# Performance work log

Hardware: AMD Instinct MI355X
Metric: run time of the kernel (lower is better)

Reference implementation:

```python
import jax, jax.numpy as jnp
import numpy as np

EMBED_DIM = 1024
NHEAD = 16
HEAD_DIM = EMBED_DIM // NHEAD
BASE = 10000.0


def rope_tables(seq_len, dim):
    # dim = head_dim; freqs over dim/2
    inv_freq = 1.0 / (BASE ** (jnp.arange(0, dim, 2, dtype=jnp.float32) / dim))
    t = jnp.arange(seq_len, dtype=jnp.float32)
    freqs = jnp.einsum('i,j->ij', t, inv_freq)          # [S, dim/2]
    return jnp.cos(freqs), jnp.sin(freqs)


def apply_rope(x, cos, sin):
    # x: [B,H,S,D]; cos/sin: [S, D/2] broadcast over B,H
    x1, x2 = jnp.split(x, 2, axis=-1)
    return jnp.concatenate((x1 * cos - x2 * sin, x1 * sin + x2 * cos), axis=-1)


def setup_inputs() -> dict:
    key = jax.random.key(0)
    ks = jax.random.split(key, 7)
    B, S, E = 2, 2048, EMBED_DIM
    scale = 1.0 / np.sqrt(E)
    return {
        'query': jax.random.normal(ks[0], (B, S, E), dtype=jnp.float32),
        'key':   jax.random.normal(ks[1], (B, S, E), dtype=jnp.float32),
        'value': jax.random.normal(ks[2], (B, S, E), dtype=jnp.float32),
        'Wq': jax.random.normal(ks[3], (E, E), dtype=jnp.float32) * scale,
        'Wk': jax.random.normal(ks[4], (E, E), dtype=jnp.float32) * scale,
        'Wv': jax.random.normal(ks[5], (E, E), dtype=jnp.float32) * scale,
        'Wo': jax.random.normal(ks[6], (E, E), dtype=jnp.float32) * scale,
    }


def reference(query, key, value, Wq, Wk, Wv, Wo):
    B, Sq, E = query.shape
    Skv = key.shape[1]
    H, D = NHEAD, HEAD_DIM
    # projections (nn.Linear: x @ W.T), split heads -> [B,H,S,D]
    q = (query @ Wq.T).reshape(B, Sq, H, D).transpose(0, 2, 1, 3)
    k = (key   @ Wk.T).reshape(B, Skv, H, D).transpose(0, 2, 1, 3)
    v = (value @ Wv.T).reshape(B, Skv, H, D).transpose(0, 2, 1, 3)
    cos, sin = rope_tables(Sq, D)
    q = apply_rope(q, cos, sin)
    k = apply_rope(k, cos, sin)
    scores = jnp.einsum('bhqd,bhkd->bhqk', q, k) / jnp.sqrt(jnp.asarray(D, q.dtype))
    probs = jax.nn.softmax(scores, axis=-1)
    out = jnp.einsum('bhqk,bhkd->bhqd', probs, v)
    out = out.transpose(0, 2, 1, 3).reshape(B, Sq, E)
    return out @ Wo.T
```

## Files before the change

kernel.cpp:

```cpp
#include <hip/hip_runtime.h>

typedef __bf16 bf16_t;
typedef __attribute__((ext_vector_type(8))) __bf16 bf16x8;
typedef __attribute__((ext_vector_type(4))) __bf16 bf16x4;
typedef __attribute__((ext_vector_type(4))) float f32x4;
typedef __attribute__((ext_vector_type(16))) float f32x16;
typedef __attribute__((ext_vector_type(4))) int i32x4;

#define GAS __attribute__((address_space(1)))
#define LAS __attribute__((address_space(3)))

#define CFENCE() asm volatile("" ::: "memory")

__device__ __forceinline__ void gload_lds16(const bf16_t* g, bf16_t* l) {
  __builtin_amdgcn_global_load_lds((const GAS char*)(const char*)g,
                                   (LAS char*)(char*)l, 16, 0, 0);
}

__global__ __launch_bounds__(256) void f2bf_w(const float* __restrict__ wq,
                                              const float* __restrict__ wk,
                                              const float* __restrict__ wv,
                                              const float* __restrict__ wo,
                                              bf16_t* __restrict__ wsb,
                                              float* __restrict__ ct,
                                              float* __restrict__ st) {
  if (blockIdx.x >= 4096) {
    const int gid = (blockIdx.x - 4096) * 256 + threadIdx.x;
    const int s = gid >> 5, j = gid & 31;
    const float inv = exp2f(-(float)j * (13.287712379549449f / 32.0f));
    const float ang = (float)s * inv;
    ct[gid] = cosf(ang);
    st[gid] = sinf(ang);
    return;
  }
  const size_t W = 1048576;
  const size_t gid = (size_t)(blockIdx.x * 256 + threadIdx.x) * 4;
  const float* src; size_t off;
  if      (gid < W)     { src = wq; off = gid; }
  else if (gid < 2 * W) { src = wk; off = gid - W; }
  else if (gid < 3 * W) { src = wv; off = gid - 2 * W; }
  else                  { src = wo; off = gid - 3 * W; }
  const float4 vv = *(const float4*)(src + off);
  bf16x4 o;
  o[0] = (bf16_t)vv.x; o[1] = (bf16_t)vv.y; o[2] = (bf16_t)vv.z; o[3] = (bf16_t)vv.w;
  *(bf16x4*)(wsb + gid) = o;
}

template <int EPI, int AF32>
__device__ __forceinline__ void gemm_bt_body(const void* __restrict__ Ap,
                                             const bf16_t* __restrict__ Bm,
                                             void* __restrict__ Cout,
                                             const float* __restrict__ ctab,
                                             const float* __restrict__ stab,
                                             const float scale,
                                             const int m0, const int n0,
                                             bf16_t* __restrict__ sm) {
  constexpr int K = 1024, N = 1024;
  bf16_t* As = sm;
  bf16_t* Bs0 = sm + 8192;
  const int tid = threadIdx.x;
  const int lane = tid & 63;
  const int w = tid >> 6;
  const int wr = w >> 1, wc = w & 1;
  const int g = lane >> 4, c = lane & 15;
  const bf16_t* Ab = (const bf16_t*)Ap;
  const float* Af = (const float*)Ap;

  f32x4 acc[4][4] = {};

  if (AF32) {
    float4 aregs[2][8];
#pragma unroll
    for (int i = 0; i < 4; ++i) {
      const int chunk0 = (i * 4 + w) * 64;
      const int idx = chunk0 + lane;
      const int row = idx >> 3;
      const int sw = (idx & 7) ^ (row & 7);
      gload_lds16(Bm + (size_t)(n0 + row) * K + sw * 8, Bs0 + chunk0 * 8);
    }
    CFENCE();
#pragma unroll
    for (int i = 0; i < 4; ++i) {
      const int idx8 = i * 256 + tid;
      const int row = idx8 >> 3, j8 = idx8 & 7;
      const size_t base = (size_t)(m0 + row) * K + j8 * 8;
      aregs[0][2 * i]     = *(const float4*)(Af + base);
      aregs[0][2 * i + 1] = *(const float4*)(Af + base + 4);
    }
    CFENCE();
#pragma unroll
    for (int i = 0; i < 4; ++i) {
      const int idx8 = i * 256 + tid;
      const int row = idx8 >> 3, j8 = idx8 & 7;
      const size_t base = (size_t)(m0 + row) * K + 64 + j8 * 8;
      aregs[1][2 * i]     = *(const float4*)(Af + base);
      aregs[1][2 * i + 1] = *(const float4*)(Af + base + 4);
    }
    asm volatile("s_waitcnt vmcnt(8)" ::: "memory");

#pragma unroll
    for (int t = 0; t < 16; ++t) {
      const int pc = t & 1;
      bf16_t* BsC = Bs0 + pc * 8192;
      bf16_t* BsN = Bs0 + (pc ^ 1) * 8192;
      if (t > 0) { __builtin_amdgcn_s_barrier(); CFENCE(); }
#pragma unroll
      for (int i = 0; i < 4; ++i) {
        const int idx8 = i * 256 + tid;
        const int row = idx8 >> 3, j8 = idx8 & 7;
        bf16x8 o;
        o[0] = (bf16_t)aregs[pc][2 * i].x;     o[1] = (bf16_t)aregs[pc][2 * i].y;
        o[2] = (bf16_t)aregs[pc][2 * i].z;     o[3] = (bf16_t)aregs[pc][2 * i].w;
        o[4] = (bf16_t)aregs[pc][2 * i + 1].x; o[5] = (bf16_t)aregs[pc][2 * i + 1].y;
        o[6] = (bf16_t)aregs[pc][2 * i + 1].z; o[7] = (bf16_t)aregs[pc][2 * i + 1].w;
        *(bf16x8*)(As + row * 64 + ((j8 ^ (row & 7)) * 8)) = o;
      }
      CFENCE();
      if (t < 15) {
#pragma unroll
        for (int i = 0; i < 4; ++i) {
          const int chunk0 = (i * 4 + w) * 64;
          const int idx = chunk0 + lane;
          const int row = idx >> 3;
          const int sw = (idx & 7) ^ (row & 7);
          gload_lds16(Bm + (size_t)(n0 + row) * K + ((t + 1) * 64 + sw * 8),
                      BsN + chunk0 * 8);
        }
      }
      CFENCE();
      if (t < 14) {
#pragma unroll
        for (int i = 0; i < 4; ++i) {
          const int idx8 = i * 256 + tid;
          const int row = idx8 >> 3, j8 = idx8 & 7;
          const size_t base = (size_t)(m0 + row) * K + (t + 2) * 64 + j8 * 8;
          aregs[pc][2 * i]     = *(const float4*)(Af + base);
          aregs[pc][2 * i + 1] = *(const float4*)(Af + base + 4);
        }
      }
      asm volatile("s_waitcnt lgkmcnt(0)" ::: "memory");
      __builtin_amdgcn_s_barrier();
      CFENCE();
      bf16x8 af[4][2], bfr[4][2];
#pragma unroll
      for (int tt = 0; tt < 4; ++tt)
#pragma unroll
        for (int kc = 0; kc < 2; ++kc) {
          const int ra = wr * 64 + tt * 16 + c;
          af[tt][kc] = *(const bf16x8*)(As + ra * 64 + (((kc * 4 + g) ^ (ra & 7)) * 8));
          const int rb = wc * 64 + tt * 16 + c;
          bfr[tt][kc] = *(const bf16x8*)(BsC + rb * 64 + (((kc * 4 + g) ^ (rb & 7)) * 8));
        }
#pragma unroll
      for (int mi = 0; mi < 4; ++mi)
#pragma unroll
        for (int ni = 0; ni < 4; ++ni)
#pragma unroll
          for (int kc = 0; kc < 2; ++kc)
            acc[mi][ni] = __builtin_amdgcn_mfma_f32_16x16x32_bf16(
                af[mi][kc], bfr[ni][kc], acc[mi][ni], 0, 0, 0);
      if (t < 14)       asm volatile("s_waitcnt vmcnt(8)" ::: "memory");
      else if (t == 14) asm volatile("s_waitcnt vmcnt(0)" ::: "memory");
    }
    __syncthreads();
  } else {
    for (int k0 = 0; k0 < K; k0 += 64) {
#pragma unroll
      for (int i = 0; i < 4; ++i) {
        const int chunk0 = (i * 4 + w) * 64;
        const int idx = chunk0 + lane;
        const int row = idx >> 3;
        const int sw = (idx & 7) ^ (row & 7);
        gload_lds16(Ab + (size_t)(m0 + row) * K + (k0 + sw * 8), As + chunk0 * 8);
        gload_lds16(Bm + (size_t)(n0 + row) * K + (k0 + sw * 8), Bs0 + chunk0 * 8);
      }
      __syncthreads();
      bf16x8 af[4][2], bfr[4][2];
#pragma unroll
      for (int tt = 0; tt < 4; ++tt)
#pragma unroll
        for (int kc = 0; kc < 2; ++kc) {
          const int ra = wr * 64 + tt * 16 + c;
          af[tt][kc] = *(const bf16x8*)(As + ra * 64 + (((kc * 4 + g) ^ (ra & 7)) * 8));
          const int rb = wc * 64 + tt * 16 + c;
          bfr[tt][kc] = *(const bf16x8*)(Bs0 + rb * 64 + (((kc * 4 + g) ^ (rb & 7)) * 8));
        }
#pragma unroll
      for (int mi = 0; mi < 4; ++mi)
#pragma unroll
        for (int ni = 0; ni < 4; ++ni)
#pragma unroll
          for (int kc = 0; kc < 2; ++kc)
            acc[mi][ni] = __builtin_amdgcn_mfma_f32_16x16x32_bf16(
                af[mi][kc], bfr[ni][kc], acc[mi][ni], 0, 0, 0);
      __syncthreads();
    }
  }

  if (EPI == 2) {
#pragma unroll
    for (int mi = 0; mi < 4; ++mi)
#pragma unroll
      for (int ni = 0; ni < 4; ++ni)
#pragma unroll
        for (int r = 0; r < 4; ++r) {
          const int lr = wr * 64 + mi * 16 + g * 4 + r;
          const int lc = wc * 64 + ni * 16 + c;
          sm[lc * 136 + lr] = (bf16_t)acc[mi][ni][r];
        }
    __syncthreads();
    bf16_t* Vt = (bf16_t*)Cout;
    const int bb = m0 >> 11, sbase = m0 & 2047;
#pragma unroll
    for (int it = 0; it < 8; ++it) {
      const int idx = it * 256 + tid;
      const int lc = idx >> 4, kk = idx & 15;
      const bf16x8 vv = *(const bf16x8*)(sm + lc * 136 + kk * 8);
      *(bf16x8*)(Vt + ((size_t)(bb * 1024 + n0 + lc)) * 2048 + sbase + kk * 8) = vv;
    }
    return;
  }
  if (EPI == 0 && ctab != nullptr) {
    bf16_t* Cb = (bf16_t*)Cout;
#pragma unroll
    for (int mi = 0; mi < 4; ++mi)
#pragma unroll
      for (int r = 0; r < 4; ++r) {
        const int grow = m0 + wr * 64 + mi * 16 + g * 4 + r;
        const int s = grow & 2047;
        const float* crow = ctab + s * 32;
        const float* srow = stab + s * 32;
#pragma unroll
        for (int ni = 0; ni < 2; ++ni) {
          const int j = ni * 16 + c;
          const float cc = crow[j], ss = srow[j];
          const float x1 = acc[mi][ni][r];
          const float x2 = acc[mi][ni + 2][r];
          const int gcol = n0 + wc * 64 + j;
          Cb[(size_t)grow * N + gcol]      = (bf16_t)((x1 * cc - x2 * ss) * scale);
          Cb[(size_t)grow * N + gcol + 32] = (bf16_t)((x1 * ss + x2 * cc) * scale);
        }
      }
    return;
  }
#pragma unroll
  for (int mi = 0; mi < 4; ++mi)
#pragma unroll
    for (int ni = 0; ni < 4; ++ni)
#pragma unroll
      for (int r = 0; r < 4; ++r) {
        const int grow = m0 + wr * 64 + mi * 16 + g * 4 + r;
        const int gcol = n0 + wc * 64 + ni * 16 + c;
        const float v = acc[mi][ni][r];
        if (EPI == 0) ((bf16_t*)Cout)[(size_t)grow * N + gcol] = (bf16_t)v;
        else          ((float*)Cout)[(size_t)grow * N + gcol] = v;
      }
}

__global__ __launch_bounds__(256) void qkv_gemm(
    const float* __restrict__ qf, const float* __restrict__ kf, const float* __restrict__ vf,
    const bf16_t* __restrict__ wqb, const bf16_t* __restrict__ wkb, const bf16_t* __restrict__ wvb,
    bf16_t* __restrict__ Qp, bf16_t* __restrict__ Kp, bf16_t* __restrict__ Vtp,
    const float* __restrict__ ctab, const float* __restrict__ stab) {
  __shared__ __align__(16) bf16_t sm[24576];
  const int bid = blockIdx.x;
  const int wg = (bid & 7) * 96 + (bid >> 3);
  const int z = wg >> 8;
  const int rem = wg & 255;
  const int m0 = (rem >> 3) * 128;
  const int n0 = (rem & 7) * 128;
  if (z == 0) {
    gemm_bt_body<0, 1>(qf, wqb, Qp, ctab, stab, 0.18033688011112042f, m0, n0, sm);
  } else if (z == 1) {
    gemm_bt_body<0, 1>(kf, wkb, Kp, ctab, stab, 1.0f, m0, n0, sm);
  } else {
    gemm_bt_body<2, 1>(vf, wvb, Vtp, nullptr, nullptr, 1.0f, m0, n0, sm);
  }
}

__global__ __launch_bounds__(256) void out_gemm(const bf16_t* __restrict__ A,
                                                const bf16_t* __restrict__ B,
                                                float* __restrict__ C) {
  __shared__ __align__(16) bf16_t sm[17408];
  const int bid = blockIdx.x;
  const int wg = (bid & 7) * 32 + (bid >> 3);
  const int m0 = (wg >> 3) * 128;
  const int n0 = (wg & 7) * 128;
  gemm_bt_body<1, 0>(A, B, C, nullptr, nullptr, 1.0f, m0, n0, sm);
}

__global__ __launch_bounds__(512, 4) void flash_attn(const bf16_t* __restrict__ Q,
                                                     const bf16_t* __restrict__ Kr,
                                                     const bf16_t* __restrict__ Vt,
                                                     bf16_t* __restrict__ O) {
  __shared__ __align__(16) bf16_t Ksm[2][2][64 * 64];
  __shared__ __align__(16) bf16_t Vsm[2][2][64 * 64];
  const int tid = threadIdx.x, lane = tid & 63, w = tid >> 6;
  const int wl = w & 3, g = w >> 2;
  const int li = lane & 31, hi = lane >> 5;
  const int bid = blockIdx.x;
  const int xcd = bid & 7, slot = bid >> 3;
  const int bh = xcd * 4 + (slot >> 4);
  const int qb = slot & 15;
  const int b = bh >> 4, h = bh & 15;
  const int q0 = qb * 128 + wl * 32;

  bf16x8 qf[4];
  {
    const size_t qaddr = ((size_t)b * 2048 + q0 + li) * 1024 + h * 64 + hi * 8;
#pragma unroll
    for (int ks = 0; ks < 4; ++ks) qf[ks] = *(const bf16x8*)(Q + qaddr + ks * 16);
  }

  bf16x8 ones;
#pragma unroll
  for (int j = 0; j < 8; ++j) ones[j] = (bf16_t)1.0f;

  const f32x16 zero16 = {};
  f32x16 o0 = zero16, o1 = zero16, osum = zero16;

  const size_t kbase  = (size_t)b * 2048 * 1024 + h * 64;
  const size_t vtbase = (size_t)((b * 16 + h) * 64) * 2048;
  const int kv_off = g * 1024;

#define STAGE(buf, kv0)                                                          \
  {                                                                              \
    _Pragma("unroll")                                                            \
    for (int i = 0; i < 2; ++i) {                                                \
      const int chunk0 = (i * 4 + wl) * 64;                                      \
      const int idx = chunk0 + lane;                                             \
      const int row = idx >> 3;                                                  \
      const int sw = ((idx & 7) ^ (row & 7)) * 8;                                \
      gload_lds16(Kr + kbase + (size_t)((kv0) + row) * 1024 + sw,                \
                  &Ksm[g][buf][chunk0 * 8]);                                     \
      gload_lds16(Vt + vtbase + (size_t)row * 2048 + (kv0) + sw,                 \
                  &Vsm[g][buf][chunk0 * 8]);                                     \
    }                                                                            \
  }

#define CVTPK(dst, lo_, hi_) \
  asm("v_cvt_pk_bf16_f32 %0, %1, %2" : "=v"(dst) : "v"(lo_), "v"(hi_))
#define PLSWAP(x_, y_) \
  asm volatile("v_permlane32_swap_b32 %0, %1" : "+v"(x_), "+v"(y_))

  STAGE(0, kv_off)
  asm volatile("s_waitcnt vmcnt(0)" ::: "memory");
  __builtin_amdgcn_s_barrier();
  int cur = 0;
  for (int t = 0; t < 16; ++t) {
    if (t < 15) STAGE(cur ^ 1, kv_off + (t + 1) * 64)

    f32x16 p0 = zero16, p1 = zero16;
    __builtin_amdgcn_s_setprio(1);
#pragma unroll
    for (int ks = 0; ks < 4; ++ks) {
      const int r0 = li;
      const bf16x8 kf0 = *(const bf16x8*)(&Ksm[g][cur][r0 * 64 + (((ks * 2 + hi) ^ (r0 & 7)) * 8)]);
      p0 = __builtin_amdgcn_mfma_f32_32x32x16_bf16(kf0, qf[ks], p0, 0, 0, 0);
      const int r1 = 32 + li;
      const bf16x8 kf1 = *(const bf16x8*)(&Ksm[g][cur][r1 * 64 + (((ks * 2 + hi) ^ (r1 & 7)) * 8)]);
      p1 = __builtin_amdgcn_mfma_f32_32x32x16_bf16(kf1, qf[ks], p1, 0, 0, 0);
    }
    __builtin_amdgcn_s_setprio(0);

#pragma unroll
    for (int j = 0; j < 16; ++j) { p0[j] = exp2f(p0[j]); p1[j] = exp2f(p1[j]); }

    bf16x8 pa[4];
#pragma unroll
    for (int ks = 0; ks < 4; ++ks) {
      int A_, B_, C_, D_;
      if (ks == 0) { CVTPK(A_, p0[0], p0[1]); CVTPK(B_, p0[2], p0[3]);
                     CVTPK(C_, p0[4], p0[5]); CVTPK(D_, p0[6], p0[7]); }
      else if (ks == 1) { CVTPK(A_, p0[8],  p0[9]);  CVTPK(B_, p0[10], p0[11]);
                          CVTPK(C_, p0[12], p0[13]); CVTPK(D_, p0[14], p0[15]); }
      else if (ks == 2) { CVTPK(A_, p1[0], p1[1]); CVTPK(B_, p1[2], p1[3]);
                          CVTPK(C_, p1[4], p1[5]); CVTPK(D_, p1[6], p1[7]); }
      else { CVTPK(A_, p1[8],  p1[9]);  CVTPK(B_, p1[10], p1[11]);
             CVTPK(C_, p1[12], p1[13]); CVTPK(D_, p1[14], p1[15]); }
      PLSWAP(A_, C_);
      PLSWAP(B_, D_);
      i32x4 iv; iv[0] = A_; iv[1] = B_; iv[2] = C_; iv[3] = D_;
      pa[ks] = __builtin_bit_cast(bf16x8, iv);
    }

    __builtin_amdgcn_s_setprio(1);
#pragma unroll
    for (int ks = 0; ks < 4; ++ks) {
      const int r0 = li;
      const bf16x8 vf0 = *(const bf16x8*)(&Vsm[g][cur][r0 * 64 + (((ks * 2 + hi) ^ (r0 & 7)) * 8)]);
      o0 = __builtin_amdgcn_mfma_f32_32x32x16_bf16(pa[ks], vf0, o0, 0, 0, 0);
      const int r1 = 32 + li;
      const bf16x8 vf1 = *(const bf16x8*)(&Vsm[g][cur][r1 * 64 + (((ks * 2 + hi) ^ (r1 & 7)) * 8)]);
      o1 = __builtin_amdgcn_mfma_f32_32x32x16_bf16(pa[ks], vf1, o1, 0, 0, 0);
      osum = __builtin_amdgcn_mfma_f32_32x32x16_bf16(pa[ks], ones, osum, 0, 0, 0);
    }
    __builtin_amdgcn_s_setprio(0);

    if (t < 15) {
      asm volatile("s_waitcnt vmcnt(0)" ::: "memory");
      __builtin_amdgcn_s_barrier();
    }
    cur ^= 1;
  }
#undef STAGE
#undef CVTPK
#undef PLSWAP

  float* Osm = (float*)&Ksm[0][0][0];
  float* lsm = (float*)&Vsm[0][0][0];

  if (g == 1) {
    float* Ow = Osm + wl * 2048;
#pragma unroll
    for (int reg = 0; reg < 16; ++reg) {
      const int ql = (reg & 3) + 8 * (reg >> 2) + 4 * hi;
      Ow[ql * 64 + li]      = o0[reg];
      Ow[ql * 64 + 32 + li] = o1[reg];
      if (li == 0) lsm[wl * 32 + ql] = osum[reg];
    }
  }
  __syncthreads();
  if (g == 0) {
    const float* Ow = Osm + wl * 2048;
#pragma unroll
    for (int reg = 0; reg < 16; ++reg) {
      const int ql = (reg & 3) + 8 * (reg >> 2) + 4 * hi;
      const float rl = 1.0f / (osum[reg] + lsm[wl * 32 + ql]);
      const size_t base = ((size_t)b * 2048 + q0 + ql) * 1024 + h * 64 + li;
      O[base]      = (bf16_t)((o0[reg] + Ow[ql * 64 + li])      * rl);
      O[base + 32] = (bf16_t)((o1[reg] + Ow[ql * 64 + 32 + li]) * rl);
    }
  }
}

extern "C" void kernel_launch(void* const* d_in, const int* in_sizes, int n_in,
                              void* d_out, int out_size, void* d_ws, size_t ws_size,
                              hipStream_t stream) {
  (void)in_sizes; (void)n_in; (void)out_size; (void)ws_size;
  const float* q_in = (const float*)d_in[0];
  const float* k_in = (const float*)d_in[1];
  const float* v_in = (const float*)d_in[2];
  const float* wq = (const float*)d_in[3];
  const float* wk = (const float*)d_in[4];
  const float* wv = (const float*)d_in[5];
  const float* wo = (const float*)d_in[6];
  float* out = (float*)d_out;

  bf16_t* ws = (bf16_t*)d_ws;
  const size_t T = 4096ull * 1024ull;
  const size_t W = 1024ull * 1024ull;
  bf16_t* wqb = ws;
  bf16_t* wkb = wqb + W;
  bf16_t* wvb = wkb + W;
  bf16_t* wob = wvb + W;
  bf16_t* Qp  = wob + W;
  bf16_t* Kp  = Qp + T;
  bf16_t* Vtp = Kp + T;
  bf16_t* AO  = Vtp + T;
  float* ctab = (float*)(AO + T);
  float* stab = ctab + 65536;

  f2bf_w<<<4352, 256, 0, stream>>>(wq, wk, wv, wo, wqb, ctab, stab);
  qkv_gemm<<<768, 256, 0, stream>>>(q_in, k_in, v_in, wqb, wkb, wvb, Qp, Kp, Vtp,
                                    ctab, stab);
  flash_attn<<<512, 512, 0, stream>>>(Qp, Kp, Vtp, AO);
  out_gemm<<<256, 256, 0, stream>>>(AO, wob, out);
}
```

Baseline: 129.9 us.

## Load K and V fragments directly from global memory instead of LDS staging

The flash attention kernel stops staging K and V tiles into double-buffered LDS via global_load_lds and instead has each wave load its MFMA fragments straight from global memory into registers. This removes the per-tile barriers and waitcnt synchronization and shrinks LDS use to the final reduction buffers. In exchange, K/V tiles are no longer shared across the four waves of a group, so global and L2 traffic rises roughly fourfold, and load latency is exposed with no explicit prefetch.

Result: slower. 191.8 us (+47.7%).

```diff
diff --git a/kernel.cpp b/kernel.cpp
--- a/kernel.cpp
+++ b/kernel.cpp
@@ -293,8 +293,8 @@
                                                      const bf16_t* __restrict__ Kr,
                                                      const bf16_t* __restrict__ Vt,
                                                      bf16_t* __restrict__ O) {
-  __shared__ __align__(16) bf16_t Ksm[2][2][64 * 64];
-  __shared__ __align__(16) bf16_t Vsm[2][2][64 * 64];
+  __shared__ float Osm[8192];
+  __shared__ float lsm[128];
   const int tid = threadIdx.x, lane = tid & 63, w = tid >> 6;
   const int wl = w & 3, g = w >> 2;
   const int li = lane & 31, hi = lane >> 5;
@@ -319,49 +319,39 @@
   const f32x16 zero16 = {};
   f32x16 o0 = zero16, o1 = zero16, osum = zero16;
 
-  const size_t kbase  = (size_t)b * 2048 * 1024 + h * 64;
-  const size_t vtbase = (size_t)((b * 16 + h) * 64) * 2048;
-  const int kv_off = g * 1024;
-
-#define STAGE(buf, kv0)                                                          \
-  {                                                                              \
-    _Pragma("unroll")                                                            \
-    for (int i = 0; i < 2; ++i) {                                                \
-      const int chunk0 = (i * 4 + wl) * 64;                                      \
-      const int idx = chunk0 + lane;                                             \
-      const int row = idx >> 3;                                                  \
-      const int sw = ((idx & 7) ^ (row & 7)) * 8;                                \
-      gload_lds16(Kr + kbase + (size_t)((kv0) + row) * 1024 + sw,                \
-                  &Ksm[g][buf][chunk0 * 8]);                                     \
-      gload_lds16(Vt + vtbase + (size_t)row * 2048 + (kv0) + sw,                 \
-                  &Vsm[g][buf][chunk0 * 8]);                                     \
-    }                                                                            \
-  }
+  const bf16_t* Kb = Kr + (size_t)b * 2048 * 1024 + h * 64 + hi * 8 +
+                     (size_t)(g * 1024 + li) * 1024;
+  const bf16_t* Vb = Vt + (size_t)((b * 16 + h) * 64) * 2048 + g * 1024 + hi * 8 +
+                     (size_t)li * 2048;
 
 #define CVTPK(dst, lo_, hi_) \
   asm("v_cvt_pk_bf16_f32 %0, %1, %2" : "=v"(dst) : "v"(lo_), "v"(hi_))
 #define PLSWAP(x_, y_) \
   asm volatile("v_permlane32_swap_b32 %0, %1" : "+v"(x_), "+v"(y_))
 
-  STAGE(0, kv_off)
-  asm volatile("s_waitcnt vmcnt(0)" ::: "memory");
-  __builtin_amdgcn_s_barrier();
-  int cur = 0;
   for (int t = 0; t < 16; ++t) {
-    if (t < 15) STAGE(cur ^ 1, kv_off + (t + 1) * 64)
+    const int kvc = t * 64;
 
     f32x16 p0 = zero16, p1 = zero16;
-    __builtin_amdgcn_s_setprio(1);
-#pragma unroll
-    for (int ks = 0; ks < 4; ++ks) {
-      const int r0 = li;
-      const bf16x8 kf0 = *(const bf16x8*)(&Ksm[g][cur][r0 * 64 + (((ks * 2 + hi) ^ (r0 & 7)) * 8)]);
-      p0 = __builtin_amdgcn_mfma_f32_32x32x16_bf16(kf0, qf[ks], p0, 0, 0, 0);
-      const int r1 = 32 + li;
-      const bf16x8 kf1 = *(const bf16x8*)(&Ksm[g][cur][r1 * 64 + (((ks * 2 + hi) ^ (r1 & 7)) * 8)]);
-      p1 = __builtin_amdgcn_mfma_f32_32x32x16_bf16(kf1, qf[ks], p1, 0, 0, 0);
-    }
-    __builtin_amdgcn_s_setprio(0);
+    {
+      bf16x8 kf[4];
+#pragma unroll
+      for (int ks = 0; ks < 4; ++ks)
+        kf[ks] = *(const bf16x8*)(Kb + (size_t)kvc * 1024 + ks * 16);
+      __builtin_amdgcn_s_setprio(1);
+#pragma unroll
+      for (int ks = 0; ks < 4; ++ks)
+        p0 = __builtin_amdgcn_mfma_f32_32x32x16_bf16(kf[ks], qf[ks], p0, 0, 0, 0);
+      __builtin_amdgcn_s_setprio(0);
+#pragma unroll
+      for (int ks = 0; ks < 4; ++ks)
+        kf[ks] = *(const bf16x8*)(Kb + (size_t)(kvc + 32) * 1024 + ks * 16);
+      __builtin_amdgcn_s_setprio(1);
+#pragma unroll
+      for (int ks = 0; ks < 4; ++ks)
+        p1 = __builtin_amdgcn_mfma_f32_32x32x16_bf16(kf[ks], qf[ks], p1, 0, 0, 0);
+      __builtin_amdgcn_s_setprio(0);
+    }
 
 #pragma unroll
     for (int j = 0; j < 16; ++j) { p0[j] = exp2f(p0[j]); p1[j] = exp2f(p1[j]); }
@@ -384,31 +374,30 @@
       pa[ks] = __builtin_bit_cast(bf16x8, iv);
     }
 
-    __builtin_amdgcn_s_setprio(1);
-#pragma unroll
-    for (int ks = 0; ks < 4; ++ks) {
-      const int r0 = li;
-      const bf16x8 vf0 = *(const bf16x8*)(&Vsm[g][cur][r0 * 64 + (((ks * 2 + hi) ^ (r0 & 7)) * 8)]);
-      o0 = __builtin_amdgcn_mfma_f32_32x32x16_bf16(pa[ks], vf0, o0, 0, 0, 0);
-      const int r1 = 32 + li;
-      const bf16x8 vf1 = *(const bf16x8*)(&Vsm[g][cur][r1 * 64 + (((ks * 2 + hi) ^ (r1 & 7)) * 8)]);
-      o1 = __builtin_amdgcn_mfma_f32_32x32x16_bf16(pa[ks], vf1, o1, 0, 0, 0);
-      osum = __builtin_amdgcn_mfma_f32_32x32x16_bf16(pa[ks], ones, osum, 0, 0, 0);
-    }
-    __builtin_amdgcn_s_setprio(0);
-
-    if (t < 15) {
-      asm volatile("s_waitcnt vmcnt(0)" ::: "memory");
-      __builtin_amdgcn_s_barrier();
-    }
-    cur ^= 1;
-  }
-#undef STAGE
+    {
+      bf16x8 vf[4];
+#pragma unroll
+      for (int ks = 0; ks < 4; ++ks)
+        vf[ks] = *(const bf16x8*)(Vb + kvc + ks * 16);
+      __builtin_amdgcn_s_setprio(1);
+#pragma unroll
+      for (int ks = 0; ks < 4; ++ks) {
+        o0 = __builtin_amdgcn_mfma_f32_32x32x16_bf16(pa[ks], vf[ks], o0, 0, 0, 0);
+        osum = __builtin_amdgcn_mfma_f32_32x32x16_bf16(pa[ks], ones, osum, 0, 0, 0);
+      }
+      __builtin_amdgcn_s_setprio(0);
+#pragma unroll
+      for (int ks = 0; ks < 4; ++ks)
+        vf[ks] = *(const bf16x8*)(Vb + (size_t)32 * 2048 + kvc + ks * 16);
+      __builtin_amdgcn_s_setprio(1);
+#pragma unroll
+      for (int ks = 0; ks < 4; ++ks)
+        o1 = __builtin_amdgcn_mfma_f32_32x32x16_bf16(pa[ks], vf[ks], o1, 0, 0, 0);
+      __builtin_amdgcn_s_setprio(0);
+    }
+  }
 #undef CVTPK
 #undef PLSWAP
-
-  float* Osm = (float*)&Ksm[0][0][0];
-  float* lsm = (float*)&Vsm[0][0][0];
 
   if (g == 1) {
     float* Ow = Osm + wl * 2048;
```

## Split flash-attn KV halves across blocks and merge partials in out-projection GEMM

Applied to the files above, without the earlier changes.

The attention kernel previously used 512-thread blocks whose two wave groups each processed half the keys and merged results through LDS. Each KV half now runs in its own 256-thread block, doubling the grid. Blocks write unnormalized fp32 partial outputs and row sums to global memory. The output GEMM's A loader reads both partials and sums, normalizes, converts to bf16 and stores into LDS, prefetching the next k-tile into registers. This removes the intra-block sync and LDS merge and adds parallelism, at the cost of writing and reading fp32 partials, roughly four times the previous bf16 AO traffic.

Result: slower. 139.5 us (+7.4%).

```diff
diff --git a/kernel.cpp b/kernel.cpp
--- a/kernel.cpp
+++ b/kernel.cpp
@@ -46,7 +46,7 @@
   *(bf16x4*)(wsb + gid) = o;
 }
 
-template <int EPI, int AF32>
+template <int EPI, int MODE>
 __device__ __forceinline__ void gemm_bt_body(const void* __restrict__ Ap,
                                              const bf16_t* __restrict__ Bm,
                                              void* __restrict__ Cout,
@@ -54,7 +54,10 @@
                                              const float* __restrict__ stab,
                                              const float scale,
                                              const int m0, const int n0,
-                                             bf16_t* __restrict__ sm) {
+                                             bf16_t* __restrict__ sm,
+                                             const float* __restrict__ A2f,
+                                             const float* __restrict__ lw0,
+                                             const float* __restrict__ lw1) {
   constexpr int K = 1024, N = 1024;
   bf16_t* As = sm;
   bf16_t* Bs0 = sm + 8192;
@@ -68,7 +71,7 @@
 
   f32x4 acc[4][4] = {};
 
-  if (AF32) {
+  if (MODE == 1) {
     float4 aregs[2][8];
 #pragma unroll
     for (int i = 0; i < 4; ++i) {
@@ -164,17 +167,71 @@
     }
     __syncthreads();
   } else {
+    float4 aregs[8], bregs[8];
+    if (MODE == 3) {
+#pragma unroll
+      for (int i = 0; i < 4; ++i) {
+        const int idx8 = i * 256 + tid;
+        const int row = idx8 >> 3, j8 = idx8 & 7;
+        const size_t base = (size_t)(m0 + row) * K + j8 * 8;
+        aregs[2 * i]     = *(const float4*)(Af + base);
+        aregs[2 * i + 1] = *(const float4*)(Af + base + 4);
+        bregs[2 * i]     = *(const float4*)(A2f + base);
+        bregs[2 * i + 1] = *(const float4*)(A2f + base + 4);
+      }
+    }
     for (int k0 = 0; k0 < K; k0 += 64) {
-#pragma unroll
-      for (int i = 0; i < 4; ++i) {
-        const int chunk0 = (i * 4 + w) * 64;
-        const int idx = chunk0 + lane;
-        const int row = idx >> 3;
-        const int sw = (idx & 7) ^ (row & 7);
-        gload_lds16(Ab + (size_t)(m0 + row) * K + (k0 + sw * 8), As + chunk0 * 8);
-        gload_lds16(Bm + (size_t)(n0 + row) * K + (k0 + sw * 8), Bs0 + chunk0 * 8);
+      if (MODE == 3) {
+        const int hk = k0 >> 6;
+#pragma unroll
+        for (int i = 0; i < 4; ++i) {
+          const int idx8 = i * 256 + tid;
+          const int row = idx8 >> 3, j8 = idx8 & 7;
+          const int lidx = (m0 + row) * 16 + hk;
+          const float rl = 1.0f / (lw0[lidx] + lw1[lidx]);
+          bf16x8 o;
+          o[0] = (bf16_t)((aregs[2 * i].x     + bregs[2 * i].x)     * rl);
+          o[1] = (bf16_t)((aregs[2 * i].y     + bregs[2 * i].y)     * rl);
+          o[2] = (bf16_t)((aregs[2 * i].z     + bregs[2 * i].z)     * rl);
+          o[3] = (bf16_t)((aregs[2 * i].w     + bregs[2 * i].w)     * rl);
+          o[4] = (bf16_t)((aregs[2 * i + 1].x + bregs[2 * i + 1].x) * rl);
+          o[5] = (bf16_t)((aregs[2 * i + 1].y + bregs[2 * i + 1].y) * rl);
+          o[6] = (bf16_t)((aregs[2 * i + 1].z + bregs[2 * i + 1].z) * rl);
+          o[7] = (bf16_t)((aregs[2 * i + 1].w + bregs[2 * i + 1].w) * rl);
+          *(bf16x8*)(As + row * 64 + ((j8 ^ (row & 7)) * 8)) = o;
+        }
+#pragma unroll
+        for (int i = 0; i < 4; ++i) {
+          const int chunk0 = (i * 4 + w) * 64;
+          const int idx = chunk0 + lane;
+          const int row = idx >> 3;
+          const int sw = (idx & 7) ^ (row & 7);
+          gload_lds16(Bm + (size_t)(n0 + row) * K + (k0 + sw * 8), Bs0 + chunk0 * 8);
+        }
+      } else {
+#pragma unroll
+        for (int i = 0; i < 4; ++i) {
+          const int chunk0 = (i * 4 + w) * 64;
+          const int idx = chunk0 + lane;
+          const int row = idx >> 3;
+          const int sw = (idx & 7) ^ (row & 7);
+          gload_lds16(Ab + (size_t)(m0 + row) * K + (k0 + sw * 8), As + chunk0 * 8);
+          gload_lds16(Bm + (size_t)(n0 + row) * K + (k0 + sw * 8), Bs0 + chunk0 * 8);
+        }
       }
       __syncthreads();
+      if (MODE == 3 && k0 + 64 < K) {
+#pragma unroll
+        for (int i = 0; i < 4; ++i) {
+          const int idx8 = i * 256 + tid;
+          const int row = idx8 >> 3, j8 = idx8 & 7;
+          const size_t base = (size_t)(m0 + row) * K + (k0 + 64) + j8 * 8;
+          aregs[2 * i]     = *(const float4*)(Af + base);
+          aregs[2 * i + 1] = *(const float4*)(Af + base + 4);
+          bregs[2 * i]     = *(const float4*)(A2f + base);
+          bregs[2 * i + 1] = *(const float4*)(A2f + base + 4);
+        }
+      }
       bf16x8 af[4][2], bfr[4][2];
 #pragma unroll
       for (int tt = 0; tt < 4; ++tt)
@@ -270,15 +327,21 @@
   const int m0 = (rem >> 3) * 128;
   const int n0 = (rem & 7) * 128;
   if (z == 0) {
-    gemm_bt_body<0, 1>(qf, wqb, Qp, ctab, stab, 0.18033688011112042f, m0, n0, sm);
+    gemm_bt_body<0, 1>(qf, wqb, Qp, ctab, stab, 0.18033688011112042f, m0, n0, sm,
+                       nullptr, nullptr, nullptr);
   } else if (z == 1) {
-    gemm_bt_body<0, 1>(kf, wkb, Kp, ctab, stab, 1.0f, m0, n0, sm);
+    gemm_bt_body<0, 1>(kf, wkb, Kp, ctab, stab, 1.0f, m0, n0, sm,
+                       nullptr, nullptr, nullptr);
   } else {
-    gemm_bt_body<2, 1>(vf, wvb, Vtp, nullptr, nullptr, 1.0f, m0, n0, sm);
-  }
-}
-
-__global__ __launch_bounds__(256) void out_gemm(const bf16_t* __restrict__ A,
+    gemm_bt_body<2, 1>(vf, wvb, Vtp, nullptr, nullptr, 1.0f, m0, n0, sm,
+                       nullptr, nullptr, nullptr);
+  }
+}
+
+__global__ __launch_bounds__(256) void out_gemm(const float* __restrict__ A1,
+                                                const float* __restrict__ A2,
+                                                const float* __restrict__ l0,
+                                                const float* __restrict__ l1,
                                                 const bf16_t* __restrict__ B,
                                                 float* __restrict__ C) {
   __shared__ __align__(16) bf16_t sm[17408];
@@ -286,24 +349,28 @@
   const int wg = (bid & 7) * 32 + (bid >> 3);
   const int m0 = (wg >> 3) * 128;
   const int n0 = (wg & 7) * 128;
-  gemm_bt_body<1, 0>(A, B, C, nullptr, nullptr, 1.0f, m0, n0, sm);
-}
-
-__global__ __launch_bounds__(512, 4) void flash_attn(const bf16_t* __restrict__ Q,
+  gemm_bt_body<1, 3>(A1, B, C, nullptr, nullptr, 1.0f, m0, n0, sm, A2, l0, l1);
+}
+
+__global__ __launch_bounds__(256, 4) void flash_attn(const bf16_t* __restrict__ Q,
                                                      const bf16_t* __restrict__ Kr,
                                                      const bf16_t* __restrict__ Vt,
-                                                     bf16_t* __restrict__ O) {
-  __shared__ __align__(16) bf16_t Ksm[2][2][64 * 64];
-  __shared__ __align__(16) bf16_t Vsm[2][2][64 * 64];
+                                                     float* __restrict__ O0,
+                                                     float* __restrict__ O1,
+                                                     float* __restrict__ l0,
+                                                     float* __restrict__ l1) {
+  __shared__ __align__(16) bf16_t Ksm[2][64 * 64];
+  __shared__ __align__(16) bf16_t Vsm[2][64 * 64];
   const int tid = threadIdx.x, lane = tid & 63, w = tid >> 6;
-  const int wl = w & 3, g = w >> 2;
   const int li = lane & 31, hi = lane >> 5;
   const int bid = blockIdx.x;
   const int xcd = bid & 7, slot = bid >> 3;
-  const int bh = xcd * 4 + (slot >> 4);
-  const int qb = slot & 15;
+  const int bh = xcd * 4 + (slot >> 5);
+  const int rem = slot & 31;
+  const int qb = rem >> 1;
+  const int g = rem & 1;
   const int b = bh >> 4, h = bh & 15;
-  const int q0 = qb * 128 + wl * 32;
+  const int q0 = qb * 128 + w * 32;
 
   bf16x8 qf[4];
   {
@@ -327,14 +394,14 @@
   {                                                                              \
     _Pragma("unroll")                                                            \
     for (int i = 0; i < 2; ++i) {                                                \
-      const int chunk0 = (i * 4 + wl) * 64;                                      \
+      const int chunk0 = (i * 4 + w) * 64;                                       \
       const int idx = chunk0 + lane;                                             \
       const int row = idx >> 3;                                                  \
       const int sw = ((idx & 7) ^ (row & 7)) * 8;                                \
       gload_lds16(Kr + kbase + (size_t)((kv0) + row) * 1024 + sw,                \
-                  &Ksm[g][buf][chunk0 * 8]);                                     \
+                  &Ksm[buf][chunk0 * 8]);                                        \
       gload_lds16(Vt + vtbase + (size_t)row * 2048 + (kv0) + sw,                 \
-                  &Vsm[g][buf][chunk0 * 8]);                                     \
+                  &Vsm[buf][chunk0 * 8]);                                        \
     }                                                                            \
   }
 
@@ -355,10 +422,10 @@
 #pragma unroll
     for (int ks = 0; ks < 4; ++ks) {
       const int r0 = li;
-      const bf16x8 kf0 = *(const bf16x8*)(&Ksm[g][cur][r0 * 64 + (((ks * 2 + hi) ^ (r0 & 7)) * 8)]);
+      const bf16x8 kf0 = *(const bf16x8*)(&Ksm[cur][r0 * 64 + (((ks * 2 + hi) ^ (r0 & 7)) * 8)]);
       p0 = __builtin_amdgcn_mfma_f32_32x32x16_bf16(kf0, qf[ks], p0, 0, 0, 0);
       const int r1 = 32 + li;
-      const bf16x8 kf1 = *(const bf16x8*)(&Ksm[g][cur][r1 * 64 + (((ks * 2 + hi) ^ (r1 & 7)) * 8)]);
+      const bf16x8 kf1 = *(const bf16x8*)(&Ksm[cur][r1 * 64 + (((ks * 2 + hi) ^ (r1 & 7)) * 8)]);
       p1 = __builtin_amdgcn_mfma_f32_32x32x16_bf16(kf1, qf[ks], p1, 0, 0, 0);
     }
     __builtin_amdgcn_s_setprio(0);
@@ -388,10 +455,10 @@
 #pragma unroll
     for (int ks = 0; ks < 4; ++ks) {
       const int r0 = li;
-      const bf16x8 vf0 = *(const bf16x8*)(&Vsm[g][cur][r0 * 64 + (((ks * 2 + hi) ^ (r0 & 7)) * 8)]);
+      const bf16x8 vf0 = *(const bf16x8*)(&Vsm[cur][r0 * 64 + (((ks * 2 + hi) ^ (r0 & 7)) * 8)]);
       o0 = __builtin_amdgcn_mfma_f32_32x32x16_bf16(pa[ks], vf0, o0, 0, 0, 0);
       const int r1 = 32 + li;
-      const bf16x8 vf1 = *(const bf16x8*)(&Vsm[g][cur][r1 * 64 + (((ks * 2 + hi) ^ (r1 & 7)) * 8)]);
+      const bf16x8 vf1 = *(const bf16x8*)(&Vsm[cur][r1 * 64 + (((ks * 2 + hi) ^ (r1 & 7)) * 8)]);
       o1 = __builtin_amdgcn_mfma_f32_32x32x16_bf16(pa[ks], vf1, o1, 0, 0, 0);
       osum = __builtin_amdgcn_mfma_f32_32x32x16_bf16(pa[ks], ones, osum, 0, 0, 0);
     }
@@ -407,30 +474,16 @@
 #undef CVTPK
 #undef PLSWAP
 
-  float* Osm = (float*)&Ksm[0][0][0];
-  float* lsm = (float*)&Vsm[0][0][0];
-
-  if (g == 1) {
-    float* Ow = Osm + wl * 2048;
-#pragma unroll
-    for (int reg = 0; reg < 16; ++reg) {
-      const int ql = (reg & 3) + 8 * (reg >> 2) + 4 * hi;
-      Ow[ql * 64 + li]      = o0[reg];
-      Ow[ql * 64 + 32 + li] = o1[reg];
-      if (li == 0) lsm[wl * 32 + ql] = osum[reg];
-    }
-  }
-  __syncthreads();
-  if (g == 0) {
-    const float* Ow = Osm + wl * 2048;
-#pragma unroll
-    for (int reg = 0; reg < 16; ++reg) {
-      const int ql = (reg & 3) + 8 * (reg >> 2) + 4 * hi;
-      const float rl = 1.0f / (osum[reg] + lsm[wl * 32 + ql]);
-      const size_t base = ((size_t)b * 2048 + q0 + ql) * 1024 + h * 64 + li;
-      O[base]      = (bf16_t)((o0[reg] + Ow[ql * 64 + li])      * rl);
-      O[base + 32] = (bf16_t)((o1[reg] + Ow[ql * 64 + 32 + li]) * rl);
-    }
+  float* Og = g ? O1 : O0;
+  float* lg = g ? l1 : l0;
+#pragma unroll
+  for (int reg = 0; reg < 16; ++reg) {
+    const int ql = (reg & 3) + 8 * (reg >> 2) + 4 * hi;
+    const size_t tok = (size_t)b * 2048 + q0 + ql;
+    const size_t base = tok * 1024 + h * 64 + li;
+    Og[base]      = o0[reg];
+    Og[base + 32] = o1[reg];
+    if (li == 0) lg[tok * 16 + h] = osum[reg];
   }
 }
 
@@ -457,13 +510,16 @@
   bf16_t* Qp  = wob + W;
   bf16_t* Kp  = Qp + T;
   bf16_t* Vtp = Kp + T;
-  bf16_t* AO  = Vtp + T;
-  float* ctab = (float*)(AO + T);
+  float* O0f  = (float*)(Vtp + T);
+  float* O1f  = O0f + T;
+  float* ctab = O1f + T;
   float* stab = ctab + 65536;
+  float* l0   = stab + 65536;
+  float* l1   = l0 + 65536;
 
   f2bf_w<<<4352, 256, 0, stream>>>(wq, wk, wv, wo, wqb, ctab, stab);
   qkv_gemm<<<768, 256, 0, stream>>>(q_in, k_in, v_in, wqb, wkb, wvb, Qp, Kp, Vtp,
                                     ctab, stab);
-  flash_attn<<<512, 512, 0, stream>>>(Qp, Kp, Vtp, AO);
-  out_gemm<<<256, 256, 0, stream>>>(AO, wob, out);
-}
+  flash_attn<<<1024, 256, 0, stream>>>(Qp, Kp, Vtp, O0f, O1f, l0, l1);
+  out_gemm<<<256, 256, 0, stream>>>(O0f, O1f, l0, l1, wob, out);
+}
```
